# Kernel tuning notes

Measured on AMD Instinct MI355X. Metric: run time of the kernel, lower is better.

Reference implementation:

```python
import jax, jax.numpy as jnp
import numpy as np

# model hyperparameters (from init_kwargs 'model' mapping)
SIG = 10.0       # kernel length scale
C = 0.0          # energy integration constant
STD = 1.0        # normalization std
M, N_ATOMS = 64, 24
T_ROWS, DESC = 6000, N_ATOMS * (N_ATOMS - 1) // 2  # 276


def setup_inputs() -> dict:
    key = jax.random.key(0)
    k1, k2, k3 = jax.random.split(key, 3)
    # spread atoms out so pairwise distances are O(1..10) Angstrom-like
    Rs = jax.random.normal(k1, (M, N_ATOMS, 3), jnp.float32) * 3.0
    # training descriptors are inverse distances -> positive values in (0,1)
    xs_train = jax.random.uniform(k2, (T_ROWS, DESC), jnp.float32)
    Jx_alphas = jax.random.normal(k3, (T_ROWS, DESC), jnp.float32) * 0.1
    return {"Rs": Rs, "xs_train": xs_train, "Jx_alphas": Jx_alphas}


def reference(Rs, xs_train, Jx_alphas):
    sig = SIG
    q = np.sqrt(5.0) / sig
    m, n = Rs.shape[0], Rs.shape[1]
    i, j = np.tril_indices(n, k=-1)  # lower-triangular atom pairs, P entries

    # pairwise coordinate differences [M, N, N, 3]
    diffs = Rs[:, :, None, :] - Rs[:, None, :, :]
    # inverse pairwise distances over tril pairs -> descriptor xs [M, P]
    d_ij = jnp.linalg.norm(diffs[:, i, j, :], axis=-1)
    xs = 1.0 / d_ij

    # descriptor differences to all (permuted) training points [M, T, P]
    x_diffs = q * xs[:, None, :] - q * xs_train[None, :, :]
    x_dists = jnp.linalg.norm(x_diffs, axis=-1)            # [M, T]
    exp_xs = (5.0 / (3.0 * sig ** 2)) * jnp.exp(-x_dists)  # [M, T]
    dot = jnp.einsum('mtp,tp->mt', x_diffs, Jx_alphas)     # [M, T]
    exp1 = exp_xs * (1.0 + x_dists)                        # [M, T]

    F1 = jnp.einsum('mt,mtp->mp', exp_xs * dot, x_diffs)   # [M, P]
    F2 = exp1 @ Jx_alphas                                  # [M, P]
    Fs_x = (F1 - F2) * xs ** 3                             # [M, P]

    # scatter pair forces back onto the symmetric [N, N] pair grid;
    # diagonal diffs are zero so leaving mult=0 there matches the original
    mult = jnp.zeros((m, n, n), Rs.dtype)
    mult = mult.at[:, i, j].set(Fs_x).at[:, j, i].set(Fs_x)
    Fs = (diffs * mult[..., None]).sum(axis=1) * STD       # [M, N, 3]

    Es = (exp1 * dot).sum(axis=-1) / q * STD + C           # [M]
    return Es, Fs
```

## Files before the change

kernel.cpp:

```cpp
#include <hip/hip_runtime.h>
#include <math.h>

#define MM 64
#define NA 24
#define NP 276
#define NT 6000
#define QC 0.22360679774997896f
#define EXPC 0.01666666666666667f

#define OFF_WT   0
#define OFF_ET   387072
#define OFF_SLAB 774144
#define OFF_ESP  1763328
#define OFF_SWP  1787328
#define OFF_XS2  1811328
#define OFF_UU   1828992
#define OFF_VV   1829056
#define OFF_C1   1835056

#define G2S   28
#define G2CH  216
#define G2R   72
#define G2_AS 68
#define G2_BS 18

__device__ __forceinline__ void p2ij(int p, int& i, int& j) {
  int ii = (int)((1.0f + sqrtf(1.0f + 8.0f * (float)p)) * 0.5f);
  while (ii * (ii - 1) / 2 > p) ii--;
  while ((ii + 1) * ii / 2 <= p) ii++;
  j = p - ii * (ii - 1) / 2;
  i = ii;
}

__global__ __launch_bounds__(256) void k_pre(const float* __restrict__ Rs,
                                             const float* __restrict__ xt,
                                             const float* __restrict__ Ja,
                                             float* __restrict__ ws) {
  const int tid = threadIdx.x;
  const int bid = blockIdx.x;
  if (bid < MM) {
    if (bid < 2) {
      float* tz = ws + (bid ? OFF_ET : OFF_WT) + (size_t)NT * 64;
      for (int z = tid; z < 48 * 64; z += 256) tz[z] = 0.f;
    }
    const int m = bid;
    __shared__ float sR[NA * 3];
    __shared__ float sAcc[4];
    if (tid < NA * 3) sR[tid] = Rs[m * NA * 3 + tid];
    __syncthreads();
    float acc = 0.f;
    for (int p = tid; p < NP; p += 256) {
      int i, j;
      p2ij(p, i, j);
      const float dx = sR[i * 3 + 0] - sR[j * 3 + 0];
      const float dy = sR[i * 3 + 1] - sR[j * 3 + 1];
      const float dz = sR[i * 3 + 2] - sR[j * 3 + 2];
      const float u = 1.0f / sqrtf(dx * dx + dy * dy + dz * dz);
      ws[OFF_XS2 + (size_t)(m >> 5) * NP * 32 + p * 32 + (m & 31)] = u;
      acc = fmaf(u, u, acc);
    }
#pragma unroll
    for (int off = 32; off; off >>= 1) acc += __shfl_down(acc, off);
    if ((tid & 63) == 0) sAcc[tid >> 6] = acc;
    __syncthreads();
    if (tid == 0) ws[OFF_UU + m] = sAcc[0] + sAcc[1] + sAcc[2] + sAcc[3];
  } else {
    const int tl = tid >> 4;
    const int l16 = tid & 15;
    const int t = (bid - MM) * 16 + tl;
    const float* xr = xt + (size_t)t * NP;
    const float* jr = Ja + (size_t)t * NP;
    float a = 0.f, b = 0.f;
#pragma unroll 4
    for (int k = l16; k < NP; k += 16) {
      const float v = xr[k];
      a = fmaf(v, v, a);
      b = fmaf(v, jr[k], b);
    }
#pragma unroll
    for (int off = 8; off; off >>= 1) {
      a += __shfl_down(a, off, 16);
      b += __shfl_down(b, off, 16);
    }
    if (l16 == 0) { ws[OFF_VV + t] = a; ws[OFF_C1 + t] = b; }
  }
}

__global__ __launch_bounds__(256, 2) void k1(const float* __restrict__ xt,
                                             const float* __restrict__ Ja,
                                             float* __restrict__ ws) {
  __shared__ __align__(16) float Bv[16 * NP];
  __shared__ __align__(16) float Bj[16 * NP];
  __shared__ __align__(16) float As[NP * 32];
  __shared__ float sEsW[4][32], sSwW[4][32];
  const int tid = threadIdx.x;
  const int t0 = blockIdx.x * 16;
  const int m0 = blockIdx.y * 32;
  const int r = tid & 15;
  const int c = tid >> 4;

  const float vvt = ws[OFF_VV + t0 + c];
  const float c1t = ws[OFF_C1 + t0 + c];
  const float2 uu2 = *(const float2*)(ws + OFF_UU + m0 + 2 * r);

  {
    const float4* xs4 = (const float4*)(xt + (size_t)t0 * NP);
    const float4* js4 = (const float4*)(Ja + (size_t)t0 * NP);
    const float4* as4 = (const float4*)(ws + OFF_XS2 + (size_t)blockIdx.y * NP * 32);
    float4* bv4 = (float4*)Bv;
    float4* bj4 = (float4*)Bj;
    float4* a4  = (float4*)As;
    for (int i = tid; i < 16 * NP / 4; i += 256) { bv4[i] = xs4[i]; bj4[i] = js4[i]; }
    for (int i = tid; i < NP * 32 / 4; i += 256) a4[i] = as4[i];
  }
  __syncthreads();

  float av0 = 0.f, av1 = 0.f, aj0 = 0.f, aj1 = 0.f;
  const float* BvR = Bv + c * NP;
  const float* BjR = Bj + c * NP;
  const float* Ac = As + 2 * r;
#pragma unroll 3
  for (int kk = 0; kk < NP; kk += 4) {
    const float4 bv = *(const float4*)(BvR + kk);
    const float4 bj = *(const float4*)(BjR + kk);
    const float2 a0 = *(const float2*)(Ac + (kk + 0) * 32);
    const float2 a1 = *(const float2*)(Ac + (kk + 1) * 32);
    const float2 a2 = *(const float2*)(Ac + (kk + 2) * 32);
    const float2 a3 = *(const float2*)(Ac + (kk + 3) * 32);
    av0 = fmaf(a0.x, bv.x, av0); aj0 = fmaf(a0.x, bj.x, aj0);
    av1 = fmaf(a0.y, bv.x, av1); aj1 = fmaf(a0.y, bj.x, aj1);
    av0 = fmaf(a1.x, bv.y, av0); aj0 = fmaf(a1.x, bj.y, aj0);
    av1 = fmaf(a1.y, bv.y, av1); aj1 = fmaf(a1.y, bj.y, aj1);
    av0 = fmaf(a2.x, bv.z, av0); aj0 = fmaf(a2.x, bj.z, aj0);
    av1 = fmaf(a2.y, bv.z, av1); aj1 = fmaf(a2.y, bj.z, aj1);
    av0 = fmaf(a3.x, bv.w, av0); aj0 = fmaf(a3.x, bj.w, aj0);
    av1 = fmaf(a3.y, bv.w, av1); aj1 = fmaf(a3.y, bj.w, aj1);
  }

  float es2[2], sw2[2], wv[2], ev[2];
#pragma unroll
  for (int i = 0; i < 2; i++) {
    const float g1v = i ? av1 : av0;
    const float g2v = i ? aj1 : aj0;
    const float uum = i ? uu2.y : uu2.x;
    float d2 = fmaxf(uum - 2.f * g1v + vvt, 0.f);
    float xd = QC * sqrtf(d2);
    float dv = QC * (g2v - c1t);
    float ex = EXPC * __expf(-xd);
    float e1v = ex * (1.f + xd);
    float w_ = ex * dv;
    wv[i] = w_; ev[i] = e1v;
    es2[i] = e1v * dv;
    sw2[i] = w_;
  }
  const int t = t0 + c;
  *(float2*)(ws + OFF_WT + (size_t)t * 64 + m0 + 2 * r) = make_float2(wv[0], wv[1]);
  *(float2*)(ws + OFF_ET + (size_t)t * 64 + m0 + 2 * r) = make_float2(ev[0], ev[1]);

#pragma unroll
  for (int i = 0; i < 2; i++) {
    es2[i] += __shfl_down(es2[i], 32); es2[i] += __shfl_down(es2[i], 16);
    sw2[i] += __shfl_down(sw2[i], 32); sw2[i] += __shfl_down(sw2[i], 16);
  }
  const int w = tid >> 6;
  if ((tid & 63) < 16) {
    sEsW[w][2 * r + 0] = es2[0]; sEsW[w][2 * r + 1] = es2[1];
    sSwW[w][2 * r + 0] = sw2[0]; sSwW[w][2 * r + 1] = sw2[1];
  }
  __syncthreads();
  if (tid < 32) {
    const float es = sEsW[0][tid] + sEsW[1][tid] + sEsW[2][tid] + sEsW[3][tid];
    const float sw = sSwW[0][tid] + sSwW[1][tid] + sSwW[2][tid] + sSwW[3][tid];
    ws[OFF_ESP + (size_t)blockIdx.x * 64 + m0 + tid] = es;
    ws[OFF_SWP + (size_t)blockIdx.x * 64 + m0 + tid] = sw;
  }
}

__global__ __launch_bounds__(256, 2) void k2(const float* __restrict__ xt,
                                             const float* __restrict__ Ja,
                                             float* __restrict__ ws) {
  __shared__ __align__(16) float Aw[G2R][G2_AS];
  __shared__ __align__(16) float Ae[G2R][G2_AS];
  __shared__ __align__(16) float2 Bvj[G2R][G2_BS];
  const int tid = threadIdx.x;
  const int p0 = blockIdx.x * 16;
  const int cid = blockIdx.y;
  const int validp = (NP - p0 < 16) ? (NP - p0) : 16;
  const int r = tid & 31;
  const int c = tid >> 5;
  float f1[2][2] = {{0.f, 0.f}, {0.f, 0.f}};
  float f2[2][2] = {{0.f, 0.f}, {0.f, 0.f}};

  for (int rnd = 0; rnd < 3; rnd++) {
    const int k0 = cid * G2CH + rnd * G2R;
    __syncthreads();
    for (int idx = tid; idx < G2R * 16; idx += 256) {
      const int k = idx >> 4;
      const int mq = (idx & 15) * 4;
      *(float4*)&Aw[k][mq] = *(const float4*)(ws + OFF_WT + (size_t)(k0 + k) * 64 + mq);
      *(float4*)&Ae[k][mq] = *(const float4*)(ws + OFF_ET + (size_t)(k0 + k) * 64 + mq);
    }
    for (int idx = tid; idx < G2R * 4; idx += 256) {
      const int k = idx >> 2;
      const int pq = (idx & 3) * 4;
      const int t = k0 + k;
      float4 v = make_float4(0.f, 0.f, 0.f, 0.f), j = v;
      if (pq < validp && t < NT) {
        v = *(const float4*)(xt + (size_t)t * NP + p0 + pq);
        j = *(const float4*)(Ja + (size_t)t * NP + p0 + pq);
      }
      *(float4*)&Bvj[k][pq]     = make_float4(v.x, j.x, v.y, j.y);
      *(float4*)&Bvj[k][pq + 2] = make_float4(v.z, j.z, v.w, j.w);
    }
    __syncthreads();
#pragma unroll 4
    for (int k = 0; k < G2R; k++) {
      const float2 aw = *(const float2*)&Aw[k][2 * r];
      const float2 ae = *(const float2*)&Ae[k][2 * r];
      const float4 b  = *(const float4*)&Bvj[k][2 * c];
      f1[0][0] = fmaf(aw.x, b.x, f1[0][0]); f1[0][1] = fmaf(aw.x, b.z, f1[0][1]);
      f1[1][0] = fmaf(aw.y, b.x, f1[1][0]); f1[1][1] = fmaf(aw.y, b.z, f1[1][1]);
      f2[0][0] = fmaf(ae.x, b.y, f2[0][0]); f2[0][1] = fmaf(ae.x, b.w, f2[0][1]);
      f2[1][0] = fmaf(ae.y, b.y, f2[1][0]); f2[1][1] = fmaf(ae.y, b.w, f2[1][1]);
    }
  }

#pragma unroll
  for (int j = 0; j < 2; j++) {
    const int pl = 2 * c + j;
    if (pl < validp) {
      const int p = p0 + pl;
      float* b1 = ws + OFF_SLAB + ((size_t)(cid * 2 + 0) * NP + p) * 64;
      float* b2 = ws + OFF_SLAB + ((size_t)(cid * 2 + 1) * NP + p) * 64;
      *(float2*)(b1 + 2 * r) = make_float2(f1[0][j], f1[1][j]);
      *(float2*)(b2 + 2 * r) = make_float2(f2[0][j], f2[1][j]);
    }
  }
}

__global__ __launch_bounds__(512) void k3(const float* __restrict__ Rs,
                                          const float* __restrict__ ws,
                                          float* __restrict__ out) {
  const int m = blockIdx.x;
  const int tid = threadIdx.x;
  __shared__ float fx[NP];
  __shared__ float sR[NA * 3];
  __shared__ float sEsw[8], sSww[8];
  __shared__ float sTot[2];
  if (tid < NA * 3) sR[tid] = Rs[m * NA * 3 + tid];

  float aE = 0.f, aS = 0.f;
  for (int tt = tid; tt < 375; tt += 512) {
    aE += ws[OFF_ESP + (size_t)tt * 64 + m];
    aS += ws[OFF_SWP + (size_t)tt * 64 + m];
  }
#pragma unroll
  for (int off = 32; off; off >>= 1) {
    aE += __shfl_down(aE, off);
    aS += __shfl_down(aS, off);
  }
  if ((tid & 63) == 0) { sEsw[tid >> 6] = aE; sSww[tid >> 6] = aS; }
  __syncthreads();
  if (tid == 0) {
    float e = 0.f, s = 0.f;
#pragma unroll
    for (int w = 0; w < 8; w++) { e += sEsw[w]; s += sSww[w]; }
    sTot[0] = e; sTot[1] = s;
    out[m] = e / QC;
  }
  __syncthreads();
  const float sw = sTot[1];

  for (int p = tid; p < NP; p += 512) {
    float f1p = 0.f, f2 = 0.f;
#pragma unroll
    for (int s = 0; s < G2S; s++) {
      f1p += ws[OFF_SLAB + ((size_t)(s * 2 + 0) * NP + p) * 64 + m];
      f2  += ws[OFF_SLAB + ((size_t)(s * 2 + 1) * NP + p) * 64 + m];
    }
    const float u = ws[OFF_XS2 + (size_t)(m >> 5) * NP * 32 + p * 32 + (m & 31)];
    const float F1 = QC * (u * sw - f1p);
    fx[p] = (F1 - f2) * u * u * u;
  }
  __syncthreads();

  if (tid < NA * 3) {
    const int a = tid / 3, cc = tid % 3;
    const float ra = sR[a * 3 + cc];
    float acc = 0.f;
    for (int b = 0; b < NA; b++) {
      if (b == a) continue;
      const int i = a > b ? a : b, j = a > b ? b : a;
      const int p = i * (i - 1) / 2 + j;
      acc += (sR[b * 3 + cc] - ra) * fx[p];
    }
    out[MM + m * NA * 3 + tid] = acc;
  }
}

extern "C" void kernel_launch(void* const* d_in, const int* in_sizes, int n_in,
                              void* d_out, int out_size, void* d_ws, size_t ws_size,
                              hipStream_t stream) {
  const float* Rs = (const float*)d_in[0];
  const float* xt = (const float*)d_in[1];
  const float* Ja = (const float*)d_in[2];
  float* out = (float*)d_out;
  float* ws = (float*)d_ws;

  k_pre<<<MM + 375, 256, 0, stream>>>(Rs, xt, Ja, ws);
  k1<<<dim3(375, 2), 256, 0, stream>>>(xt, Ja, ws);
  k2<<<dim3(18, G2S), 256, 0, stream>>>(xt, Ja, ws);
  k3<<<MM, 512, 0, stream>>>(Rs, ws, out);
}
```

Baseline: 129.8 us.

## Widen k2 split-K grid, add separate slab reduction kernel, wave-per-row precompute

k2 now splits the training dimension into 56 chunks of 108 rows with a single load phase instead of 28 chunks processed in three rounds, doubling its grid to fill more CUs. A new k_red kernel sums the partial slabs in parallel, so k3 no longer does a strided 28-way serial reduction per output and runs with 320 threads. The precompute branch of k_pre assigns one wave per training row with coalesced loads. The cost is an extra kernel launch, twice the slab workspace traffic, and more k2 partials to sum.

```diff
diff --git a/kernel.cpp b/kernel.cpp
--- a/kernel.cpp
+++ b/kernel.cpp
@@ -8,21 +8,20 @@
 #define QC 0.22360679774997896f
 #define EXPC 0.01666666666666667f
 
+#define G2S   56
+#define G2R   108
+
 #define OFF_WT   0
 #define OFF_ET   387072
 #define OFF_SLAB 774144
-#define OFF_ESP  1763328
-#define OFF_SWP  1787328
-#define OFF_XS2  1811328
-#define OFF_UU   1828992
-#define OFF_VV   1829056
-#define OFF_C1   1835056
-
-#define G2S   28
-#define G2CH  216
-#define G2R   72
-#define G2_AS 68
-#define G2_BS 18
+#define OFF_ESP  2752512
+#define OFF_SWP  2776512
+#define OFF_XS2  2800512
+#define OFF_UU   2818176
+#define OFF_VV   2818240
+#define OFF_C1   2824240
+#define OFF_F    2830240
+#define SLABSTRIDE 35328
 
 __device__ __forceinline__ void p2ij(int p, int& i, int& j) {
   int ii = (int)((1.0f + sqrtf(1.0f + 8.0f * (float)p)) * 0.5f);
@@ -65,24 +64,31 @@
     __syncthreads();
     if (tid == 0) ws[OFF_UU + m] = sAcc[0] + sAcc[1] + sAcc[2] + sAcc[3];
   } else {
-    const int tl = tid >> 4;
-    const int l16 = tid & 15;
-    const int t = (bid - MM) * 16 + tl;
+    const int sb = bid - MM;
+    const int t = sb * 4 + (tid >> 6);
+    const int lane = tid & 63;
     const float* xr = xt + (size_t)t * NP;
     const float* jr = Ja + (size_t)t * NP;
     float a = 0.f, b = 0.f;
-#pragma unroll 4
-    for (int k = l16; k < NP; k += 16) {
-      const float v = xr[k];
+#pragma unroll
+    for (int q = 0; q < 4; q++) {
+      const float v = xr[lane + 64 * q];
+      const float jj = jr[lane + 64 * q];
       a = fmaf(v, v, a);
-      b = fmaf(v, jr[k], b);
-    }
-#pragma unroll
-    for (int off = 8; off; off >>= 1) {
-      a += __shfl_down(a, off, 16);
-      b += __shfl_down(b, off, 16);
-    }
-    if (l16 == 0) { ws[OFF_VV + t] = a; ws[OFF_C1 + t] = b; }
+      b = fmaf(v, jj, b);
+    }
+    if (lane < NP - 256) {
+      const float v = xr[256 + lane];
+      const float jj = jr[256 + lane];
+      a = fmaf(v, v, a);
+      b = fmaf(v, jj, b);
+    }
+#pragma unroll
+    for (int off = 32; off; off >>= 1) {
+      a += __shfl_down(a, off);
+      b += __shfl_down(b, off);
+    }
+    if (lane == 0) { ws[OFF_VV + t] = a; ws[OFF_C1 + t] = b; }
   }
 }
 
@@ -179,50 +185,49 @@
 __global__ __launch_bounds__(256, 2) void k2(const float* __restrict__ xt,
                                              const float* __restrict__ Ja,
                                              float* __restrict__ ws) {
-  __shared__ __align__(16) float Aw[G2R][G2_AS];
-  __shared__ __align__(16) float Ae[G2R][G2_AS];
-  __shared__ __align__(16) float2 Bvj[G2R][G2_BS];
+  __shared__ __align__(16) float Aw[G2R * 64];
+  __shared__ __align__(16) float Ae[G2R * 64];
+  __shared__ __align__(16) float2 Bvj[G2R][18];
   const int tid = threadIdx.x;
   const int p0 = blockIdx.x * 16;
   const int cid = blockIdx.y;
+  const int k0 = cid * G2R;
   const int validp = (NP - p0 < 16) ? (NP - p0) : 16;
   const int r = tid & 31;
   const int c = tid >> 5;
+
+  {
+    const float4* aws = (const float4*)(ws + OFF_WT + (size_t)k0 * 64);
+    const float4* aes = (const float4*)(ws + OFF_ET + (size_t)k0 * 64);
+    float4* aw4 = (float4*)Aw;
+    float4* ae4 = (float4*)Ae;
+    for (int idx = tid; idx < G2R * 16; idx += 256) { aw4[idx] = aws[idx]; ae4[idx] = aes[idx]; }
+  }
+  for (int idx = tid; idx < G2R * 4; idx += 256) {
+    const int k = idx >> 2;
+    const int pq = (idx & 3) * 4;
+    const int t = k0 + k;
+    float4 v = make_float4(0.f, 0.f, 0.f, 0.f), j = v;
+    if (pq < validp && t < NT) {
+      v = *(const float4*)(xt + (size_t)t * NP + p0 + pq);
+      j = *(const float4*)(Ja + (size_t)t * NP + p0 + pq);
+    }
+    *(float4*)&Bvj[k][pq]     = make_float4(v.x, j.x, v.y, j.y);
+    *(float4*)&Bvj[k][pq + 2] = make_float4(v.z, j.z, v.w, j.w);
+  }
+  __syncthreads();
+
   float f1[2][2] = {{0.f, 0.f}, {0.f, 0.f}};
   float f2[2][2] = {{0.f, 0.f}, {0.f, 0.f}};
-
-  for (int rnd = 0; rnd < 3; rnd++) {
-    const int k0 = cid * G2CH + rnd * G2R;
-    __syncthreads();
-    for (int idx = tid; idx < G2R * 16; idx += 256) {
-      const int k = idx >> 4;
-      const int mq = (idx & 15) * 4;
-      *(float4*)&Aw[k][mq] = *(const float4*)(ws + OFF_WT + (size_t)(k0 + k) * 64 + mq);
-      *(float4*)&Ae[k][mq] = *(const float4*)(ws + OFF_ET + (size_t)(k0 + k) * 64 + mq);
-    }
-    for (int idx = tid; idx < G2R * 4; idx += 256) {
-      const int k = idx >> 2;
-      const int pq = (idx & 3) * 4;
-      const int t = k0 + k;
-      float4 v = make_float4(0.f, 0.f, 0.f, 0.f), j = v;
-      if (pq < validp && t < NT) {
-        v = *(const float4*)(xt + (size_t)t * NP + p0 + pq);
-        j = *(const float4*)(Ja + (size_t)t * NP + p0 + pq);
-      }
-      *(float4*)&Bvj[k][pq]     = make_float4(v.x, j.x, v.y, j.y);
-      *(float4*)&Bvj[k][pq + 2] = make_float4(v.z, j.z, v.w, j.w);
-    }
-    __syncthreads();
 #pragma unroll 4
-    for (int k = 0; k < G2R; k++) {
-      const float2 aw = *(const float2*)&Aw[k][2 * r];
-      const float2 ae = *(const float2*)&Ae[k][2 * r];
-      const float4 b  = *(const float4*)&Bvj[k][2 * c];
-      f1[0][0] = fmaf(aw.x, b.x, f1[0][0]); f1[0][1] = fmaf(aw.x, b.z, f1[0][1]);
-      f1[1][0] = fmaf(aw.y, b.x, f1[1][0]); f1[1][1] = fmaf(aw.y, b.z, f1[1][1]);
-      f2[0][0] = fmaf(ae.x, b.y, f2[0][0]); f2[0][1] = fmaf(ae.x, b.w, f2[0][1]);
-      f2[1][0] = fmaf(ae.y, b.y, f2[1][0]); f2[1][1] = fmaf(ae.y, b.w, f2[1][1]);
-    }
+  for (int k = 0; k < G2R; k++) {
+    const float2 aw = *(const float2*)&Aw[k * 64 + 2 * r];
+    const float2 ae = *(const float2*)&Ae[k * 64 + 2 * r];
+    const float4 b  = *(const float4*)&Bvj[k][2 * c];
+    f1[0][0] = fmaf(aw.x, b.x, f1[0][0]); f1[0][1] = fmaf(aw.x, b.z, f1[0][1]);
+    f1[1][0] = fmaf(aw.y, b.x, f1[1][0]); f1[1][1] = fmaf(aw.y, b.z, f1[1][1]);
+    f2[0][0] = fmaf(ae.x, b.y, f2[0][0]); f2[0][1] = fmaf(ae.x, b.w, f2[0][1]);
+    f2[1][0] = fmaf(ae.y, b.y, f2[1][0]); f2[1][1] = fmaf(ae.y, b.w, f2[1][1]);
   }
 
 #pragma unroll
@@ -238,19 +243,28 @@
   }
 }
 
-__global__ __launch_bounds__(512) void k3(const float* __restrict__ Rs,
+__global__ __launch_bounds__(128) void k_red(float* __restrict__ ws) {
+  const int inner = blockIdx.x * 128 + threadIdx.x;
+  const float* src = ws + OFF_SLAB + inner;
+  float s = 0.f;
+#pragma unroll
+  for (int cid = 0; cid < G2S; cid++) s += src[(size_t)cid * SLABSTRIDE];
+  ws[OFF_F + inner] = s;
+}
+
+__global__ __launch_bounds__(320) void k3(const float* __restrict__ Rs,
                                           const float* __restrict__ ws,
                                           float* __restrict__ out) {
   const int m = blockIdx.x;
   const int tid = threadIdx.x;
   __shared__ float fx[NP];
   __shared__ float sR[NA * 3];
-  __shared__ float sEsw[8], sSww[8];
+  __shared__ float sEsw[5], sSww[5];
   __shared__ float sTot[2];
   if (tid < NA * 3) sR[tid] = Rs[m * NA * 3 + tid];
 
   float aE = 0.f, aS = 0.f;
-  for (int tt = tid; tt < 375; tt += 512) {
+  for (int tt = tid; tt < 375; tt += 320) {
     aE += ws[OFF_ESP + (size_t)tt * 64 + m];
     aS += ws[OFF_SWP + (size_t)tt * 64 + m];
   }
@@ -264,20 +278,16 @@
   if (tid == 0) {
     float e = 0.f, s = 0.f;
 #pragma unroll
-    for (int w = 0; w < 8; w++) { e += sEsw[w]; s += sSww[w]; }
+    for (int w = 0; w < 5; w++) { e += sEsw[w]; s += sSww[w]; }
     sTot[0] = e; sTot[1] = s;
     out[m] = e / QC;
   }
   __syncthreads();
   const float sw = sTot[1];
 
-  for (int p = tid; p < NP; p += 512) {
-    float f1p = 0.f, f2 = 0.f;
-#pragma unroll
-    for (int s = 0; s < G2S; s++) {
-      f1p += ws[OFF_SLAB + ((size_t)(s * 2 + 0) * NP + p) * 64 + m];
-      f2  += ws[OFF_SLAB + ((size_t)(s * 2 + 1) * NP + p) * 64 + m];
-    }
+  for (int p = tid; p < NP; p += 320) {
+    const float f1p = ws[OFF_F + (size_t)0 * NP * 64 + p * 64 + m];
+    const float f2  = ws[OFF_F + (size_t)1 * NP * 64 + p * 64 + m];
     const float u = ws[OFF_XS2 + (size_t)(m >> 5) * NP * 32 + p * 32 + (m & 31)];
     const float F1 = QC * (u * sw - f1p);
     fx[p] = (F1 - f2) * u * u * u;
@@ -307,8 +317,9 @@
   float* out = (float*)d_out;
   float* ws = (float*)d_ws;
 
-  k_pre<<<MM + 375, 256, 0, stream>>>(Rs, xt, Ja, ws);
+  k_pre<<<MM + 1500, 256, 0, stream>>>(Rs, xt, Ja, ws);
   k1<<<dim3(375, 2), 256, 0, stream>>>(xt, Ja, ws);
   k2<<<dim3(18, G2S), 256, 0, stream>>>(xt, Ja, ws);
-  k3<<<MM, 512, 0, stream>>>(Rs, ws, out);
-}
+  k_red<<<NP * 2, 128, 0, stream>>>(ws);
+  k3<<<MM, 320, 0, stream>>>(Rs, ws, out);
+}
```

New measurement: 118.2 us. -8.9%, faster.
